# Kernel tuning notes

Measured on AMD Instinct MI355X. Metric: run time of the kernel, lower is better.

## Reference

```python
import jax, jax.numpy as jnp
import numpy as np

N_NODES = 50000
N_EDGES = 800000
NFEAT, NHID, NCLASS = 512, 128, 40


def setup_inputs() -> dict:
    key = jax.random.key(0)
    ks = jax.random.split(key, 8)
    stdv1 = 1.0 / np.sqrt(NHID)
    stdv2 = 1.0 / np.sqrt(NCLASS)
    x = jax.random.normal(ks[0], (N_NODES, NFEAT), dtype=jnp.float32)
    W1 = jax.random.uniform(ks[1], (NFEAT, NHID), jnp.float32, -stdv1, stdv1)
    b1 = jax.random.uniform(ks[2], (NHID,), jnp.float32, -stdv1, stdv1)
    W2 = jax.random.uniform(ks[3], (NHID, NCLASS), jnp.float32, -stdv2, stdv2)
    b2 = jax.random.uniform(ks[4], (NCLASS,), jnp.float32, -stdv2, stdv2)
    edge_src = jax.random.randint(ks[5], (N_EDGES,), 0, N_NODES, dtype=jnp.int32)
    edge_dst = jax.random.randint(ks[6], (N_EDGES,), 0, N_NODES, dtype=jnp.int32)
    # normalized adjacency weights (positive, ~1/deg scale)
    edge_w = jax.random.uniform(ks[7], (N_EDGES,), jnp.float32, 0.0, 2.0 / 16.0)
    return {"x": x, "W1": W1, "b1": b1, "W2": W2, "b2": b2,
            "edge_src": edge_src, "edge_dst": edge_dst, "edge_w": edge_w}


def _spmm(edge_src, edge_dst, edge_w, support, n_nodes):
    # out[i] = sum_{e: dst(e)=i} w_e * support[src(e)]  == spmm(adj, support)
    msgs = edge_w[:, None] * support[edge_src]          # [E, F]
    return jax.ops.segment_sum(msgs, edge_dst, num_segments=n_nodes)


def reference(x, W1, b1, W2, b2, edge_src, edge_dst, edge_w):
    # layer 1: dense transform then sparse aggregation, bias, relu
    support = x @ W1                                     # [N, nhid]
    h = _spmm(edge_src, edge_dst, edge_w, support, x.shape[0]) + b1
    h = jax.nn.relu(h)
    # dropout is identity in eval mode
    # layer 2
    support2 = h @ W2                                    # [N, nclass]
    out = _spmm(edge_src, edge_dst, edge_w, support2, x.shape[0]) + b2
    return out
```

## Files before the change

### kernel.cpp

```cpp
#include <hip/hip_runtime.h>
#include <hip/hip_bf16.h>


#define NFEAT 512
#define NHID  128
#define NCLS  40
#define BSH   8
#define SLOTSH 6
#define BSLOT 6144
#define ACHUNK 2048

typedef __attribute__((ext_vector_type(8))) short bf16x8;
typedef __attribute__((ext_vector_type(4))) short bf16x4;
typedef __attribute__((ext_vector_type(4))) float f32x4;

__device__ inline short f2bf(float f) {
  __hip_bfloat16 b = __float2bfloat16(f);
  return *reinterpret_cast<short*>(&b);
}

__device__ inline bf16x8 cvt8(float4 a, float4 b) {
  bf16x8 r;
  r[0] = f2bf(a.x); r[1] = f2bf(a.y); r[2] = f2bf(a.z); r[3] = f2bf(a.w);
  r[4] = f2bf(b.x); r[5] = f2bf(b.y); r[6] = f2bf(b.z); r[7] = f2bf(b.w);
  return r;
}

__global__ __launch_bounds__(256) void zero_kernel(int4* __restrict__ p, int n4) {
  int i = blockIdx.x * 256 + threadIdx.x;
  if (i < n4) p[i] = make_int4(0, 0, 0, 0);
}

__global__ __launch_bounds__(256) void hist_kernel(
    const int* __restrict__ edst, int* __restrict__ deg, int E) {
  int e = blockIdx.x * 256 + threadIdx.x;
  if (e < E) atomicAdd(&deg[edst[e]], 1);
}

__global__ __launch_bounds__(256) void bucketize(
    const int* __restrict__ esrc, const int* __restrict__ edst,
    const float* __restrict__ ew, int* __restrict__ bcur,
    int* __restrict__ bsrc, float* __restrict__ bw, int* __restrict__ bdst,
    int E, int nb) {
  __shared__ int lh[256], lo[256], gbase[256];
  __shared__ int s_src[ACHUNK];
  __shared__ float s_w[ACHUNK];
  __shared__ int s_dst[ACHUNK];
  const int tid = threadIdx.x;
  const int base = blockIdx.x * ACHUNK;
  const int cnt = min(ACHUNK, E - base);

  for (int t = tid; t < nb; t += 256) lh[t] = 0;
  __syncthreads();

  int my_s[8], my_d[8], my_t[8];
  float my_w[8];
#pragma unroll
  for (int i = 0; i < 8; ++i) {
    int idx = base + i * 256 + tid;
    if (idx < E) {
      my_s[i] = esrc[idx];
      my_d[i] = edst[idx];
      my_w[i] = ew[idx];
      my_t[i] = atomicAdd(&lh[my_d[i] >> BSH], 1);
    }
  }
  __syncthreads();
  if (tid == 0) {
    int run = 0;
    for (int b = 0; b < nb; ++b) { lo[b] = run; run += lh[b]; }
  }
  __syncthreads();
  if (tid < nb && lh[tid] > 0)
    gbase[tid] = tid * BSLOT + atomicAdd(&bcur[tid], lh[tid]);
  __syncthreads();
#pragma unroll
  for (int i = 0; i < 8; ++i) {
    int idx = base + i * 256 + tid;
    if (idx < E) {
      int p = lo[my_d[i] >> BSH] + my_t[i];
      s_src[p] = my_s[i];
      s_w[p] = my_w[i];
      s_dst[p] = my_d[i];
    }
  }
  __syncthreads();
  for (int j = tid; j < cnt; j += 256) {
    int d = s_dst[j];
    int b = d >> BSH;
    int g = gbase[b] + (j - lo[b]);
    bsrc[g] = s_src[j];
    bw[g] = s_w[j];
    bdst[g] = d;
  }
}

__global__ __launch_bounds__(256) void bucket_scatter(
    const int* __restrict__ bcur, const int* __restrict__ bsrc,
    const float* __restrict__ bw, const int* __restrict__ bdst,
    int2* __restrict__ cwsrc, int n) {
  __shared__ int cur[1 << BSH];
  const int tid = threadIdx.x;
  const int d0 = blockIdx.x << BSH;
  for (int t = tid; t < (1 << BSH); t += 256) cur[t] = (d0 + t) << SLOTSH;
  __syncthreads();
  const int bstart = blockIdx.x * BSLOT;
  const int bend = bstart + bcur[blockIdx.x];
  for (int j = bstart + tid; j < bend; j += 256) {
    int d = bdst[j];
    int slot = atomicAdd(&cur[d - d0], 1);
    cwsrc[slot] = make_int2(bsrc[j], __float_as_int(bw[j]));
  }
}

__global__ __launch_bounds__(256) void w1t_kernel(
    const float* __restrict__ W1, __hip_bfloat16* __restrict__ W1t) {
  __shared__ float t[64][129];
  const int tid = threadIdx.x;
  const int k0 = blockIdx.x * 64;
#pragma unroll
  for (int i = 0; i < 8; ++i) {
    int f = i * 256 + tid;
    int r = f >> 5, c = (f & 31) << 2;
    float4 v = *(const float4*)&W1[(size_t)(k0 + r) * NHID + c];
    t[r][c] = v.x; t[r][c + 1] = v.y; t[r][c + 2] = v.z; t[r][c + 3] = v.w;
  }
  __syncthreads();
#pragma unroll
  for (int i = 0; i < 32; ++i) {
    int o = i * 256 + tid;
    int k = o & 63, n = o >> 6;
    W1t[(size_t)n * NFEAT + k0 + k] = __float2bfloat16(t[k][n]);
  }
}

__global__ __launch_bounds__(256, 3) void gemm1_mfma(
    const float* __restrict__ x, const __hip_bfloat16* __restrict__ W1t,
    __hip_bfloat16* __restrict__ support, int nrows) {
  __shared__ __align__(16) char sA[2][64 * 64 * 2];
  __shared__ __align__(16) char sB[2][128 * 64 * 2];
  const int tid = threadIdx.x;
  const int lane = tid & 63;
  const int wid = tid >> 6;
  const int wm = wid >> 1, wn = wid & 1;
  const int row0 = blockIdx.x * 64;
  const int l15 = lane & 15, l4 = lane >> 4;

  const int s_ar = tid >> 2;
  const int s_ac = (tid & 3) * 16;
  const int s_br = tid >> 1;
  const int s_bc = (tid & 1) * 32;
  const bool a_ok = (row0 + s_ar) < nrows;
  const float* aptr = &x[(size_t)(row0 + s_ar) * NFEAT + s_ac];
  const uint4* bptr = (const uint4*)&W1t[(size_t)s_br * NFEAT + s_bc];

  f32x4 acc[2][4];
#pragma unroll
  for (int m = 0; m < 2; ++m)
#pragma unroll
    for (int n = 0; n < 4; ++n) acc[m][n] = (f32x4){0.f, 0.f, 0.f, 0.f};

  float4 ra0[4], ra1[4];
  uint4 rb0[4], rb1[4];

  auto LOADAB = [&](int kt, int sel) {
    if (sel == 0) {
      if (a_ok) {
        const float4* p = (const float4*)(aptr + (size_t)kt * 64);
#pragma unroll
        for (int i = 0; i < 4; ++i) ra0[i] = p[i];
      } else {
        float4 z = make_float4(0.f, 0.f, 0.f, 0.f);
#pragma unroll
        for (int i = 0; i < 4; ++i) ra0[i] = z;
      }
      const uint4* q = bptr + (size_t)kt * 8;
#pragma unroll
      for (int i = 0; i < 4; ++i) rb0[i] = q[i];
    } else {
      if (a_ok) {
        const float4* p = (const float4*)(aptr + (size_t)kt * 64);
#pragma unroll
        for (int i = 0; i < 4; ++i) ra1[i] = p[i];
      } else {
        float4 z = make_float4(0.f, 0.f, 0.f, 0.f);
#pragma unroll
        for (int i = 0; i < 4; ++i) ra1[i] = z;
      }
      const uint4* q = bptr + (size_t)kt * 8;
#pragma unroll
      for (int i = 0; i < 4; ++i) rb1[i] = q[i];
    }
  };
  auto WRITE = [&](int buf, int sel) {
    bf16x8 c0, c1;
    if (sel == 0) { c0 = cvt8(ra0[0], ra0[1]); c1 = cvt8(ra0[2], ra0[3]); }
    else          { c0 = cvt8(ra1[0], ra1[1]); c1 = cvt8(ra1[2], ra1[3]); }
    int swa = (s_ar & 7) << 4;
    *(bf16x8*)(sA[buf] + ((s_ar * 128 + s_ac * 2) ^ swa)) = c0;
    *(bf16x8*)(sA[buf] + ((s_ar * 128 + s_ac * 2 + 16) ^ swa)) = c1;
    int swb = (s_br & 7) << 4;
#pragma unroll
    for (int i = 0; i < 4; ++i) {
      uint4 v = (sel == 0) ? rb0[i] : rb1[i];
      *(uint4*)(sB[buf] + ((s_br * 128 + s_bc * 2 + i * 16) ^ swb)) = v;
    }
  };
  auto COMP = [&](int buf) {
#pragma unroll
    for (int kk = 0; kk < 64; kk += 32) {
      bf16x8 a[2], b[4];
      int cb = (kk + l4 * 8) * 2;
#pragma unroll
      for (int m = 0; m < 2; ++m) {
        int r = wm * 32 + m * 16 + l15;
        a[m] = *(const bf16x8*)(sA[buf] + ((r * 128 + cb) ^ ((r & 7) << 4)));
      }
#pragma unroll
      for (int n = 0; n < 4; ++n) {
        int r = wn * 64 + n * 16 + l15;
        b[n] = *(const bf16x8*)(sB[buf] + ((r * 128 + cb) ^ ((r & 7) << 4)));
      }
#pragma unroll
      for (int m = 0; m < 2; ++m)
#pragma unroll
        for (int n = 0; n < 4; ++n)
          acc[m][n] = __builtin_amdgcn_mfma_f32_16x16x32_bf16(a[m], b[n], acc[m][n], 0, 0, 0);
    }
  };
  auto BAR = [&]() {
    asm volatile("s_waitcnt lgkmcnt(0)" ::: "memory");
    __builtin_amdgcn_sched_barrier(0);
    __builtin_amdgcn_s_barrier();
    __builtin_amdgcn_sched_barrier(0);
  };

  LOADAB(0, 0);
  LOADAB(1, 1);
  WRITE(0, 0);
  LOADAB(2, 0);
  BAR();

#pragma unroll
  for (int t = 0; t < 8; ++t) {
    if (t < 7) {
      if ((t + 1) & 1) {
        WRITE(1, 1);
        if (t + 3 < 8) LOADAB(t + 3, 1);
      } else {
        WRITE(0, 0);
        if (t + 3 < 8) LOADAB(t + 3, 0);
      }
    }
    COMP(t & 1);
    if (t < 7) BAR();
  }

#pragma unroll
  for (int m = 0; m < 2; ++m) {
#pragma unroll
    for (int r = 0; r < 4; ++r) {
      int grow = row0 + wm * 32 + m * 16 + l4 * 4 + r;
      if (grow < nrows) {
#pragma unroll
        for (int n = 0; n < 4; ++n) {
          int col = wn * 64 + n * 16 + l15;
          support[(size_t)grow * NHID + col] = __float2bfloat16(acc[m][n][r]);
        }
      }
    }
  }
}

__device__ inline void bf2unpack(unsigned int u, float& lo, float& hi) {
  union { unsigned int ui; float f; } a, b;
  a.ui = (u & 0xffffu) << 16;
  b.ui = u & 0xffff0000u;
  lo = a.f; hi = b.f;
}

__global__ __launch_bounds__(256) void spmm1_fused(
    const int* __restrict__ deg, const int2* __restrict__ cwsrc,
    const __hip_bfloat16* __restrict__ support, const float* __restrict__ b1,
    const float* __restrict__ W2, __hip_bfloat16* __restrict__ s2, int n) {
  __shared__ float swt[128 * 40];
  __shared__ float shh[4][128];
  const int tid = threadIdx.x;
  for (int i = tid; i < 128 * 40; i += 256) swt[i] = W2[i];
  __syncthreads();

  int w = tid >> 6;
  int node = blockIdx.x * 4 + w;
  int f2 = tid & 63;
  if (node >= n) return;
  int beg = node << SLOTSH;
  int end = beg + deg[node];
  float a0 = 0.f, a1 = 0.f;
  const unsigned int* sp = (const unsigned int*)support;
  int i = beg;
  for (; i + 3 < end; i += 4) {
    int2 e0 = cwsrc[i], e1 = cwsrc[i + 1], e2 = cwsrc[i + 2], e3 = cwsrc[i + 3];
    unsigned int u0 = sp[(size_t)e0.x * 64 + f2];
    unsigned int u1 = sp[(size_t)e1.x * 64 + f2];
    unsigned int u2 = sp[(size_t)e2.x * 64 + f2];
    unsigned int u3 = sp[(size_t)e3.x * 64 + f2];
    float lo, hi;
    float w0 = __int_as_float(e0.y), w1 = __int_as_float(e1.y);
    float w2 = __int_as_float(e2.y), w3 = __int_as_float(e3.y);
    bf2unpack(u0, lo, hi); a0 += w0 * lo; a1 += w0 * hi;
    bf2unpack(u1, lo, hi); a0 += w1 * lo; a1 += w1 * hi;
    bf2unpack(u2, lo, hi); a0 += w2 * lo; a1 += w2 * hi;
    bf2unpack(u3, lo, hi); a0 += w3 * lo; a1 += w3 * hi;
  }
  for (; i < end; ++i) {
    int2 e = cwsrc[i];
    float w_ = __int_as_float(e.y);
    unsigned int u = sp[(size_t)e.x * 64 + f2];
    float lo, hi;
    bf2unpack(u, lo, hi);
    a0 += w_ * lo; a1 += w_ * hi;
  }
  shh[w][f2 * 2] = fmaxf(a0 + b1[f2 * 2], 0.f);
  shh[w][f2 * 2 + 1] = fmaxf(a1 + b1[f2 * 2 + 1], 0.f);
  if (f2 < NCLS) {
    float acc = 0.f;
#pragma unroll 8
    for (int k = 0; k < 128; ++k) acc += shh[w][k] * swt[k * 40 + f2];
    s2[(size_t)node * NCLS + f2] = __float2bfloat16(acc);
  }
}

__global__ __launch_bounds__(256) void spmm2_gather(
    const int* __restrict__ deg, const int2* __restrict__ cwsrc,
    const __hip_bfloat16* __restrict__ s2,
    const float* __restrict__ b2, float* __restrict__ out, int n) {
  int node = blockIdx.x * 8 + (threadIdx.x >> 5);
  int f2 = threadIdx.x & 31;
  if (node >= n || f2 >= 20) return;
  int beg = node << SLOTSH;
  int end = beg + deg[node];
  float a0 = 0.f, a1 = 0.f;
  const unsigned int* sp = (const unsigned int*)s2;
  int i = beg;
  for (; i + 3 < end; i += 4) {
    int2 e0 = cwsrc[i], e1 = cwsrc[i + 1], e2 = cwsrc[i + 2], e3 = cwsrc[i + 3];
    unsigned int u0 = sp[(size_t)e0.x * 20 + f2];
    unsigned int u1 = sp[(size_t)e1.x * 20 + f2];
    unsigned int u2 = sp[(size_t)e2.x * 20 + f2];
    unsigned int u3 = sp[(size_t)e3.x * 20 + f2];
    float lo, hi;
    float w0 = __int_as_float(e0.y), w1 = __int_as_float(e1.y);
    float w2 = __int_as_float(e2.y), w3 = __int_as_float(e3.y);
    bf2unpack(u0, lo, hi); a0 += w0 * lo; a1 += w0 * hi;
    bf2unpack(u1, lo, hi); a0 += w1 * lo; a1 += w1 * hi;
    bf2unpack(u2, lo, hi); a0 += w2 * lo; a1 += w2 * hi;
    bf2unpack(u3, lo, hi); a0 += w3 * lo; a1 += w3 * hi;
  }
  for (; i < end; ++i) {
    int2 e = cwsrc[i];
    float w = __int_as_float(e.y);
    unsigned int u = sp[(size_t)e.x * 20 + f2];
    float lo, hi;
    bf2unpack(u, lo, hi);
    a0 += w * lo; a1 += w * hi;
  }
  float2 o;
  o.x = a0 + b2[f2 * 2];
  o.y = a1 + b2[f2 * 2 + 1];
  *(float2*)&out[(size_t)node * NCLS + f2 * 2] = o;
}

extern "C" void kernel_launch(void* const* d_in, const int* in_sizes, int n_in,
                              void* d_out, int out_size, void* d_ws, size_t ws_size,
                              hipStream_t stream) {
  const float* x   = (const float*)d_in[0];
  const float* W1  = (const float*)d_in[1];
  const float* b1  = (const float*)d_in[2];
  const float* W2  = (const float*)d_in[3];
  const float* b2  = (const float*)d_in[4];
  const int* esrc  = (const int*)d_in[5];
  const int* edst  = (const int*)d_in[6];
  const float* ew  = (const float*)d_in[7];
  float* out = (float*)d_out;

  const int N = in_sizes[0] / NFEAT;
  const int E = in_sizes[5];
  const int NB = (N + (1 << BSH) - 1) >> BSH;

  char* ws = (char*)d_ws;
  size_t off = 0;
  auto alloc = [&](size_t bytes) {
    void* p = ws + off;
    off += (bytes + 255) & ~(size_t)255;
    return p;
  };
  int2*  cwsrc = (int2*)alloc((size_t)N * (1 << SLOTSH) * 8);
  int*   degb  = (int*)alloc((size_t)((N + NB + 3) & ~3) * 4);
  int*   deg   = degb;
  int*   bcur  = degb + N;
  int*   bsrc  = (int*)alloc((size_t)NB * BSLOT * 4);
  float* bw    = (float*)alloc((size_t)NB * BSLOT * 4);
  int*   bdst  = (int*)alloc((size_t)NB * BSLOT * 4);
  __hip_bfloat16* W1t     = (__hip_bfloat16*)alloc((size_t)NHID * NFEAT * 2);
  __hip_bfloat16* support = (__hip_bfloat16*)alloc((size_t)N * NHID * 2);
  __hip_bfloat16* s2      = (__hip_bfloat16*)alloc((size_t)N * NCLS * 2);

  const int nz4 = (N + NB + 3) / 4;
  zero_kernel<<<(nz4 + 255) / 256, 256, 0, stream>>>((int4*)degb, nz4);
  hist_kernel<<<(E + 255) / 256, 256, 0, stream>>>(edst, deg, E);
  bucketize<<<(E + ACHUNK - 1) / ACHUNK, 256, 0, stream>>>(
      esrc, edst, ew, bcur, bsrc, bw, bdst, E, NB);
  bucket_scatter<<<NB, 256, 0, stream>>>(bcur, bsrc, bw, bdst, cwsrc, N);

  w1t_kernel<<<NFEAT / 64, 256, 0, stream>>>(W1, W1t);
  gemm1_mfma<<<(N + 63) / 64, 256, 0, stream>>>(x, W1t, support, N);
  spmm1_fused<<<(N + 3) / 4, 256, 0, stream>>>(deg, cwsrc, support, b1, W2, s2, N);

  spmm2_gather<<<(N + 7) / 8, 256, 0, stream>>>(deg, cwsrc, s2, b2, out, N);
}
```

Baseline: 193.9 us.

## Load edge lists once per wave and broadcast with readlane; use fp16 dot2 for W2

```diff
diff --git a/kernel.cpp b/kernel.cpp
--- a/kernel.cpp
+++ b/kernel.cpp
@@ -13,6 +13,7 @@
 typedef __attribute__((ext_vector_type(8))) short bf16x8;
 typedef __attribute__((ext_vector_type(4))) short bf16x4;
 typedef __attribute__((ext_vector_type(4))) float f32x4;
+typedef __fp16 f16x2 __attribute__((ext_vector_type(2)));
 
 __device__ inline short f2bf(float f) {
   __hip_bfloat16 b = __float2bfloat16(f);
@@ -25,6 +26,9 @@
   r[4] = f2bf(b.x); r[5] = f2bf(b.y); r[6] = f2bf(b.z); r[7] = f2bf(b.w);
   return r;
 }
+
+__device__ inline unsigned h2u(f16x2 v) { union { f16x2 h; unsigned u; } x; x.h = v; return x.u; }
+__device__ inline f16x2 u2h(unsigned u) { union { f16x2 h; unsigned u; } x; x.u = u; return x.h; }
 
 __global__ __launch_bounds__(256) void zero_kernel(int4* __restrict__ p, int n4) {
   int i = blockIdx.x * 256 + threadIdx.x;
@@ -272,60 +276,59 @@
   }
 }
 
-__device__ inline void bf2unpack(unsigned int u, float& lo, float& hi) {
-  union { unsigned int ui; float f; } a, b;
-  a.ui = (u & 0xffffu) << 16;
-  b.ui = u & 0xffff0000u;
-  lo = a.f; hi = b.f;
-}
-
 __global__ __launch_bounds__(256) void spmm1_fused(
     const int* __restrict__ deg, const int2* __restrict__ cwsrc,
     const __hip_bfloat16* __restrict__ support, const float* __restrict__ b1,
     const float* __restrict__ W2, __hip_bfloat16* __restrict__ s2, int n) {
-  __shared__ float swt[128 * 40];
-  __shared__ float shh[4][128];
+  __shared__ unsigned swt2[64 * 40];
+  __shared__ unsigned shh2[4][64];
   const int tid = threadIdx.x;
-  for (int i = tid; i < 128 * 40; i += 256) swt[i] = W2[i];
-  __syncthreads();
-
-  int w = tid >> 6;
-  int node = blockIdx.x * 4 + w;
-  int f2 = tid & 63;
+  for (int i = tid; i < 64 * 40; i += 256) {
+    int k2 = i / 40, c = i - k2 * 40;
+    swt2[i] = h2u(__builtin_amdgcn_cvt_pkrtz(W2[(2 * k2) * NCLS + c],
+                                             W2[(2 * k2 + 1) * NCLS + c]));
+  }
+  __syncthreads();
+
+  const int w = tid >> 6;
+  const int f2 = tid & 63;
+  const int node = blockIdx.x * 4 + w;
   if (node >= n) return;
-  int beg = node << SLOTSH;
-  int end = beg + deg[node];
+  const int dg = deg[node];
+  const int2 eself = cwsrc[(node << SLOTSH) + f2];
   float a0 = 0.f, a1 = 0.f;
-  const unsigned int* sp = (const unsigned int*)support;
-  int i = beg;
-  for (; i + 3 < end; i += 4) {
-    int2 e0 = cwsrc[i], e1 = cwsrc[i + 1], e2 = cwsrc[i + 2], e3 = cwsrc[i + 3];
-    unsigned int u0 = sp[(size_t)e0.x * 64 + f2];
-    unsigned int u1 = sp[(size_t)e1.x * 64 + f2];
-    unsigned int u2 = sp[(size_t)e2.x * 64 + f2];
-    unsigned int u3 = sp[(size_t)e3.x * 64 + f2];
-    float lo, hi;
-    float w0 = __int_as_float(e0.y), w1 = __int_as_float(e1.y);
-    float w2 = __int_as_float(e2.y), w3 = __int_as_float(e3.y);
-    bf2unpack(u0, lo, hi); a0 += w0 * lo; a1 += w0 * hi;
-    bf2unpack(u1, lo, hi); a0 += w1 * lo; a1 += w1 * hi;
-    bf2unpack(u2, lo, hi); a0 += w2 * lo; a1 += w2 * hi;
-    bf2unpack(u3, lo, hi); a0 += w3 * lo; a1 += w3 * hi;
-  }
-  for (; i < end; ++i) {
-    int2 e = cwsrc[i];
-    float w_ = __int_as_float(e.y);
-    unsigned int u = sp[(size_t)e.x * 64 + f2];
-    float lo, hi;
-    bf2unpack(u, lo, hi);
-    a0 += w_ * lo; a1 += w_ * hi;
-  }
-  shh[w][f2 * 2] = fmaxf(a0 + b1[f2 * 2], 0.f);
-  shh[w][f2 * 2 + 1] = fmaxf(a1 + b1[f2 * 2 + 1], 0.f);
+  const unsigned* sp = (const unsigned*)support;
+  int j = 0;
+#pragma unroll 4
+  for (; j + 3 < dg; j += 4) {
+#pragma unroll
+    for (int q = 0; q < 4; ++q) {
+      int s = __builtin_amdgcn_readlane(eself.x, j + q);
+      float wj = __int_as_float(__builtin_amdgcn_readlane(eself.y, j + q));
+      unsigned u = sp[((unsigned)s << 6) | (unsigned)f2];
+      float lo = __int_as_float(u << 16);
+      float hi = __int_as_float(u & 0xffff0000u);
+      a0 += wj * lo;
+      a1 += wj * hi;
+    }
+  }
+  for (; j < dg; ++j) {
+    int s = __builtin_amdgcn_readlane(eself.x, j);
+    float wj = __int_as_float(__builtin_amdgcn_readlane(eself.y, j));
+    unsigned u = sp[((unsigned)s << 6) | (unsigned)f2];
+    float lo = __int_as_float(u << 16);
+    float hi = __int_as_float(u & 0xffff0000u);
+    a0 += wj * lo;
+    a1 += wj * hi;
+  }
+  a0 = fmaxf(a0 + b1[f2 * 2], 0.f);
+  a1 = fmaxf(a1 + b1[f2 * 2 + 1], 0.f);
+  shh2[w][f2] = h2u(__builtin_amdgcn_cvt_pkrtz(a0, a1));
   if (f2 < NCLS) {
     float acc = 0.f;
 #pragma unroll 8
-    for (int k = 0; k < 128; ++k) acc += shh[w][k] * swt[k * 40 + f2];
+    for (int k2 = 0; k2 < 64; ++k2)
+      acc = __builtin_amdgcn_fdot2(u2h(shh2[w][k2]), u2h(swt2[k2 * 40 + f2]), acc, false);
     s2[(size_t)node * NCLS + f2] = __float2bfloat16(acc);
   }
 }
@@ -334,40 +337,44 @@
     const int* __restrict__ deg, const int2* __restrict__ cwsrc,
     const __hip_bfloat16* __restrict__ s2,
     const float* __restrict__ b2, float* __restrict__ out, int n) {
-  int node = blockIdx.x * 8 + (threadIdx.x >> 5);
-  int f2 = threadIdx.x & 31;
-  if (node >= n || f2 >= 20) return;
-  int beg = node << SLOTSH;
-  int end = beg + deg[node];
+  const int w = threadIdx.x >> 6;
+  const int f2 = threadIdx.x & 63;
+  const int node = blockIdx.x * 4 + w;
+  if (node >= n) return;
+  const int dg = deg[node];
+  const int2 eself = cwsrc[(node << SLOTSH) + f2];
+  const unsigned f2c = (f2 < 20) ? (unsigned)f2 : 0u;
   float a0 = 0.f, a1 = 0.f;
-  const unsigned int* sp = (const unsigned int*)s2;
-  int i = beg;
-  for (; i + 3 < end; i += 4) {
-    int2 e0 = cwsrc[i], e1 = cwsrc[i + 1], e2 = cwsrc[i + 2], e3 = cwsrc[i + 3];
-    unsigned int u0 = sp[(size_t)e0.x * 20 + f2];
-    unsigned int u1 = sp[(size_t)e1.x * 20 + f2];
-    unsigned int u2 = sp[(size_t)e2.x * 20 + f2];
-    unsigned int u3 = sp[(size_t)e3.x * 20 + f2];
-    float lo, hi;
-    float w0 = __int_as_float(e0.y), w1 = __int_as_float(e1.y);
-    float w2 = __int_as_float(e2.y), w3 = __int_as_float(e3.y);
-    bf2unpack(u0, lo, hi); a0 += w0 * lo; a1 += w0 * hi;
-    bf2unpack(u1, lo, hi); a0 += w1 * lo; a1 += w1 * hi;
-    bf2unpack(u2, lo, hi); a0 += w2 * lo; a1 += w2 * hi;
-    bf2unpack(u3, lo, hi); a0 += w3 * lo; a1 += w3 * hi;
-  }
-  for (; i < end; ++i) {
-    int2 e = cwsrc[i];
-    float w = __int_as_float(e.y);
-    unsigned int u = sp[(size_t)e.x * 20 + f2];
-    float lo, hi;
-    bf2unpack(u, lo, hi);
-    a0 += w * lo; a1 += w * hi;
-  }
-  float2 o;
-  o.x = a0 + b2[f2 * 2];
-  o.y = a1 + b2[f2 * 2 + 1];
-  *(float2*)&out[(size_t)node * NCLS + f2 * 2] = o;
+  const unsigned* sp = (const unsigned*)s2;
+  int j = 0;
+#pragma unroll 4
+  for (; j + 3 < dg; j += 4) {
+#pragma unroll
+    for (int q = 0; q < 4; ++q) {
+      int s = __builtin_amdgcn_readlane(eself.x, j + q);
+      float wj = __int_as_float(__builtin_amdgcn_readlane(eself.y, j + q));
+      unsigned u = sp[(unsigned)s * 20u + f2c];
+      float lo = __int_as_float(u << 16);
+      float hi = __int_as_float(u & 0xffff0000u);
+      a0 += wj * lo;
+      a1 += wj * hi;
+    }
+  }
+  for (; j < dg; ++j) {
+    int s = __builtin_amdgcn_readlane(eself.x, j);
+    float wj = __int_as_float(__builtin_amdgcn_readlane(eself.y, j));
+    unsigned u = sp[(unsigned)s * 20u + f2c];
+    float lo = __int_as_float(u << 16);
+    float hi = __int_as_float(u & 0xffff0000u);
+    a0 += wj * lo;
+    a1 += wj * hi;
+  }
+  if (f2 < 20) {
+    float2 o;
+    o.x = a0 + b2[f2 * 2];
+    o.y = a1 + b2[f2 * 2 + 1];
+    *(float2*)&out[(size_t)node * NCLS + f2 * 2] = o;
+  }
 }
 
 extern "C" void kernel_launch(void* const* d_in, const int* in_sizes, int n_in,
@@ -416,5 +423,5 @@
   gemm1_mfma<<<(N + 63) / 64, 256, 0, stream>>>(x, W1t, support, N);
   spmm1_fused<<<(N + 3) / 4, 256, 0, stream>>>(deg, cwsrc, support, b1, W2, s2, N);
 
-  spmm2_gather<<<(N + 7) / 8, 256, 0, stream>>>(deg, cwsrc, s2, b2, out, N);
-}
+  spmm2_gather<<<(N + 3) / 4, 256, 0, stream>>>(deg, cwsrc, s2, b2, out, N);
+}
```

After: 182.7 us. 5.8% less time.
